# Performance work log

Hardware: AMD Instinct MI355X
Metric: run time of the kernel (lower is better)

Reference implementation:

```python
import jax, jax.numpy as jnp
import numpy as np

NUM_FEATURES = 512
NUM_HEADS = 8
DIM_PER_HEAD = NUM_FEATURES // NUM_HEADS


def setup_inputs() -> dict:
    key = jax.random.key(0)
    ks = jax.random.split(key, 9)
    B, C, H, W = 8, NUM_FEATURES, 32, 32
    # xavier_uniform bound for 1x1 conv: sqrt(6/(fan_in+fan_out)) = sqrt(6/(2C))
    bound = float(np.sqrt(6.0 / (2.0 * C)))
    # conv bias default init: U(-1/sqrt(fan_in), 1/sqrt(fan_in))
    bbound = float(1.0 / np.sqrt(C))
    return {
        "query": jax.random.normal(ks[0], (B, C, H, W), jnp.float32),
        "key": jax.random.normal(ks[1], (B, C, H, W), jnp.float32),
        "value": jax.random.normal(ks[2], (B, C, H, W), jnp.float32),
        "wq": jax.random.uniform(ks[3], (C, C), jnp.float32, -bound, bound),
        "bq": jax.random.uniform(ks[4], (C,), jnp.float32, -bbound, bbound),
        "wk": jax.random.uniform(ks[5], (C, C), jnp.float32, -bound, bound),
        "bk": jax.random.uniform(ks[6], (C,), jnp.float32, -bbound, bbound),
        "wv": jax.random.uniform(ks[7], (C, C), jnp.float32, -bound, bound),
        "bv": jax.random.uniform(ks[8], (C,), jnp.float32, -bbound, bbound),
    }


def _proj(x, w, b):
    # 1x1 conv == per-pixel linear over channels. x: [B,C,H,W], w: [Cout,Cin]
    return jnp.einsum('oi,bihw->bohw', w, x) + b[None, :, None, None]


def _split_heads(x, nh, d):
    B, C, H, W = x.shape
    # view (B, nh, d, H*W) then permute -> (B, nh, S, d)
    return x.reshape(B, nh, d, H * W).transpose(0, 1, 3, 2)


def reference(query, key, value, wq, bq, wk, bk, wv, bv):
    B, C, H, W = query.shape
    nh, d = NUM_HEADS, DIM_PER_HEAD
    q = _split_heads(_proj(query, wq, bq), nh, d)   # [B,nh,S,d]
    k = _split_heads(_proj(key, wk, bk), nh, d)
    v = _split_heads(_proj(value, wv, bv), nh, d)
    scores = jnp.einsum('bhsd,bhtd->bhst', q, k) / jnp.sqrt(jnp.float32(d))
    attn = jax.nn.softmax(scores, axis=-1)          # [B,nh,S,S]
    out = jnp.einsum('bhst,bhtd->bhsd', attn, v)    # [B,nh,S,d]
    # combine_heads (faithful to torch): permute to (B,S,nh,d), flat reshape
    out = out.transpose(0, 2, 1, 3)                 # [B,S,nh,d]
    return out.reshape(B, C, H, W)
```

## Files before the change

### kernel.cpp

```cpp
#include <hip/hip_runtime.h>
#include <hip/hip_bf16.h>
#include <stdint.h>


typedef __attribute__((ext_vector_type(4))) float f32x4;
typedef __attribute__((ext_vector_type(8))) short short8;
typedef __attribute__((ext_vector_type(4))) unsigned int u32x4;

#define GLB_AS(p) ((const __attribute__((address_space(1))) void*)(p))
#define LDS_AS(p) ((__attribute__((address_space(3))) void*)(p))

__device__ __forceinline__ unsigned short f2b(float f) {
  unsigned int x = __builtin_bit_cast(unsigned int, f);
  x = (x + 0x7FFFu + ((x >> 16) & 1u)) >> 16;
  return (unsigned short)x;
}

__device__ __forceinline__ float exp2_hw(float x) {
  float r;
  asm("v_exp_f32 %0, %1" : "=v"(r) : "v"(x));
  return r;
}

__device__ __forceinline__ unsigned int cvtpk(float lo, float hi) {
  unsigned int r;
  asm("v_cvt_pk_bf16_f32 %0, %1, %2" : "=v"(r) : "v"(lo), "v"(hi));
  return r;
}

__device__ __forceinline__ f32x4 mfma16(short8 a, short8 b, f32x4 c) {
  return __builtin_amdgcn_mfma_f32_16x16x32_bf16(a, b, c, 0, 0, 0);
}

__global__ __launch_bounds__(256) void prep_all(const float* __restrict__ Xq,
                                                const float* __restrict__ Xk,
                                                const float* __restrict__ Xv,
                                                const float* __restrict__ wq,
                                                const float* __restrict__ wk,
                                                const float* __restrict__ wv,
                                                unsigned short* __restrict__ Xt,
                                                unsigned short* __restrict__ WO) {
  __shared__ float t[64][65];
  const int tid = threadIdx.x;
  if (blockIdx.z == 24) {
    const int bid = blockIdx.y * 16 + blockIdx.x;
#pragma unroll
    for (int k = 0; k < 6; ++k) {
      int i = bid * 1536 + k * 256 + tid;
      int which = i >> 16, off = i & 65535;
      const float* W = (which == 0) ? wq : ((which == 1) ? wk : wv);
      float4 v = ((const float4*)W)[off];
      uint2 u;
      u.x = (unsigned)f2b(v.x) | ((unsigned)f2b(v.y) << 16);
      u.y = (unsigned)f2b(v.z) | ((unsigned)f2b(v.w) << 16);
      ((uint2*)(WO + (long)which * 262144))[off] = u;
    }
    return;
  }
  const int which = blockIdx.z >> 3, bb = blockIdx.z & 7;
  const float* X = (which == 0) ? Xq : ((which == 1) ? Xk : Xv);
  const int s0 = blockIdx.x * 64, c0 = blockIdx.y * 64;
  const float* Xb = X + (long)bb * 512 * 1024;
  const int col4 = (tid & 15) * 4;
  const int r0 = tid >> 4;
#pragma unroll
  for (int it = 0; it < 4; ++it) {
    int r = r0 + it * 16;
    const float4 v = *(const float4*)&Xb[(long)(c0 + r) * 1024 + s0 + col4];
    t[r][col4 + 0] = v.x; t[r][col4 + 1] = v.y; t[r][col4 + 2] = v.z; t[r][col4 + 3] = v.w;
  }
  __syncthreads();
  const int s = tid >> 2;
  const int cp = (tid & 3) * 16;
  unsigned int u[8];
#pragma unroll
  for (int i = 0; i < 8; ++i) {
    unsigned int lo = f2b(t[cp + 2 * i][s]);
    unsigned int hi = f2b(t[cp + 2 * i + 1][s]);
    u[i] = lo | (hi << 16);
  }
  unsigned short* dst = Xt + (long)which * 8 * 1024 * 512 +
                        ((long)bb * 1024 + s0 + s) * 512 + c0 + cp;
  ((uint4*)dst)[0] = make_uint4(u[0], u[1], u[2], u[3]);
  ((uint4*)dst)[1] = make_uint4(u[4], u[5], u[6], u[7]);
}

__global__ __launch_bounds__(256, 2) void gemm_proj(
    const unsigned short* __restrict__ XT, const unsigned short* __restrict__ W3,
    unsigned short* __restrict__ QKV, const float* __restrict__ bq,
    const float* __restrict__ bk, const float* __restrict__ bv) {
  __shared__ __align__(16) unsigned short lA[128 * 64];
  __shared__ __align__(16) unsigned short lB[128 * 64];
  const long SC = 1024L * 512;
  const int bid = blockIdx.x;
  const int kind = bid >> 8;
  const int rr = bid & 255;
  const int batch = rr >> 5, tile = rr & 31;
  const unsigned short *Ab, *Bb;
  unsigned short* Cb;
  const float* bias;
  int m0, n0, N, biasN;
  float scale = 1.0f;
  if (kind < 2) {
    m0 = (tile >> 2) * 128; n0 = (tile & 3) * 128; N = 512; biasN = 1;
    Ab = XT + ((long)kind * 8 + batch) * SC;
    Bb = W3 + (long)kind * 262144;
    Cb = QKV + ((long)kind * 8 + batch) * SC;
    bias = kind ? bk : bq;
    if (kind == 0) scale = 0.18033688011112042f;
  } else {
    m0 = (tile >> 3) * 128; n0 = (tile & 7) * 128; N = 1024; biasN = 0;
    Ab = W3 + 2 * 262144;
    Bb = XT + (16L + batch) * SC;
    Cb = QKV + (16L + batch) * SC;
    bias = bv;
  }
  const int tid = threadIdx.x, lane = tid & 63, wid = tid >> 6;
  const int wr = wid >> 1, wc = wid & 1;
  const int lm = lane & 15, lg = lane >> 4;
  f32x4 acc[4][4] = {};
  for (int k0 = 0; k0 < 512; k0 += 64) {
#pragma unroll
    for (int ch = wid; ch < 16; ch += 4) {
      int e = ch * 512 + lane * 8;
      int r = e >> 6, cc = e & 63;
      __builtin_amdgcn_global_load_lds(GLB_AS(Ab + (long)(m0 + r) * 512 + k0 + cc),
                                       LDS_AS(lA + ch * 512), 16, 0, 0);
      __builtin_amdgcn_global_load_lds(GLB_AS(Bb + (long)(n0 + r) * 512 + k0 + cc),
                                       LDS_AS(lB + ch * 512), 16, 0, 0);
    }
    __syncthreads();
#pragma unroll
    for (int kk = 0; kk < 2; ++kk) {
      short8 af[4], bf[4];
#pragma unroll
      for (int i = 0; i < 4; ++i)
        af[i] = *(const short8*)&lA[(wr * 64 + i * 16 + lm) * 64 + kk * 32 + 8 * lg];
#pragma unroll
      for (int j = 0; j < 4; ++j)
        bf[j] = *(const short8*)&lB[(wc * 64 + j * 16 + lm) * 64 + kk * 32 + 8 * lg];
#pragma unroll
      for (int i = 0; i < 4; ++i)
#pragma unroll
        for (int j = 0; j < 4; ++j)
          acc[i][j] = mfma16(af[i], bf[j], acc[i][j]);
    }
    __syncthreads();
  }
#pragma unroll
  for (int i = 0; i < 4; ++i)
#pragma unroll
    for (int j = 0; j < 4; ++j)
#pragma unroll
      for (int r = 0; r < 4; ++r) {
        int m = m0 + wr * 64 + i * 16 + lg * 4 + r;
        int n = n0 + wc * 64 + j * 16 + lm;
        float bvv = biasN ? bias[n] : bias[m];
        Cb[(long)m * N + n] = f2b((acc[i][j][r] + bvv) * scale);
      }
}

__global__ __launch_bounds__(256, 2) void attn(
    const unsigned short* __restrict__ Qt, const unsigned short* __restrict__ Kt,
    const unsigned short* __restrict__ V, float* __restrict__ Out) {
  __shared__ __align__(16) unsigned short lK[2][128 * 64];
  __shared__ __align__(16) unsigned short lV[2][64 * 128];
  const int flat = blockIdx.x;
  const int xcd = flat & 7, j = flat >> 3;
  const int pair = xcd * 8 + (j >> 3);
  const int st = j & 7;
  const int b = pair >> 3, h = pair & 7;
  const int tid = threadIdx.x, lane = tid & 63, w = tid >> 6;
  const int lm = lane & 15, lg = lane >> 4;
  const int s0 = st * 128 + w * 32;
  const unsigned short* Qb = Qt + ((long)b * 1024 + s0) * 512 + h * 64;
  const unsigned short* Kb = Kt + (long)b * 1024 * 512 + h * 64;
  const unsigned short* Vb = V + ((long)b * 512 + h * 64) * 1024;

  const int kscol = ((lane & 7) ^ (lane >> 3)) * 8;
  auto stage = [&](int buf, int t0) {
#pragma unroll
    for (int jj = 0; jj < 4; ++jj) {
      int ch = w * 4 + jj;
      int krow = ch * 8 + (lane >> 3);
      __builtin_amdgcn_global_load_lds(GLB_AS(Kb + (long)(t0 + krow) * 512 + kscol),
                                       LDS_AS(&lK[buf][ch * 512]), 16, 0, 0);
      int vrow = ch * 4 + (lane >> 4);
      int vcb = (lane & 15) ^ (vrow & 15);
      __builtin_amdgcn_global_load_lds(GLB_AS(Vb + (long)vrow * 1024 + t0 + vcb * 8),
                                       LDS_AS(&lV[buf][ch * 512]), 16, 0, 0);
    }
  };

  short8 qf[2][2];
#pragma unroll
  for (int si = 0; si < 2; ++si)
#pragma unroll
    for (int kk = 0; kk < 2; ++kk)
      qf[si][kk] = *(const short8*)&Qb[(si * 16 + lm) * 512 + kk * 32 + 8 * lg];

  f32x4 o[2][4] = {};
  float lsum[2] = {};

  stage(0, 0);
  __syncthreads();

#pragma unroll 1
  for (int t = 0; t < 8; ++t) {
    const int cur = t & 1;
    if (t < 7) stage(cur ^ 1, (t + 1) * 128);
    f32x4 s[2][8] = {};
    __builtin_amdgcn_s_setprio(1);
#pragma unroll
    for (int tj = 0; tj < 8; ++tj) {
      short8 kf0 = *(const short8*)&lK[cur][(tj * 16 + lm) * 64 + 8 * (lg ^ (lm & 7))];
      short8 kf1 = *(const short8*)&lK[cur][(tj * 16 + lm) * 64 + 8 * ((lg + 4) ^ (lm & 7))];
#pragma unroll
      for (int si = 0; si < 2; ++si) {
        s[si][tj] = mfma16(kf0, qf[si][0], s[si][tj]);
        s[si][tj] = mfma16(kf1, qf[si][1], s[si][tj]);
      }
    }
    __builtin_amdgcn_s_setprio(0);
#pragma unroll
    for (int si = 0; si < 2; ++si)
#pragma unroll
      for (int tj = 0; tj < 8; ++tj)
#pragma unroll
        for (int r = 0; r < 4; ++r) {
          float p = exp2_hw(s[si][tj][r]);
          s[si][tj][r] = p;
          lsum[si] += p;
        }
#pragma unroll
    for (int tk = 0; tk < 4; ++tk) {
      short8 pa[2];
#pragma unroll
      for (int si = 0; si < 2; ++si) {
        unsigned int X01 = cvtpk(s[si][2 * tk][0], s[si][2 * tk][1]);
        unsigned int X23 = cvtpk(s[si][2 * tk][2], s[si][2 * tk][3]);
        unsigned int Y01 = cvtpk(s[si][2 * tk + 1][0], s[si][2 * tk + 1][1]);
        unsigned int Y23 = cvtpk(s[si][2 * tk + 1][2], s[si][2 * tk + 1][3]);
        asm("v_permlane32_swap_b32 %0, %1" : "+v"(X01), "+v"(Y01));
        asm("v_permlane32_swap_b32 %0, %1" : "+v"(X23), "+v"(Y23));
        asm("v_permlane16_swap_b32 %0, %1" : "+v"(X01), "+v"(Y01));
        asm("v_permlane16_swap_b32 %0, %1" : "+v"(X23), "+v"(Y23));
        u32x4 pw;
        pw[0] = X01;
        pw[1] = X23;
        pw[2] = Y01;
        pw[3] = Y23;
        pa[si] = __builtin_bit_cast(short8, pw);
      }
      __builtin_amdgcn_s_setprio(1);
#pragma unroll
      for (int dj = 0; dj < 4; ++dj) {
        short8 vf = *(const short8*)&lV[cur][(dj * 16 + lm) * 128 + 8 * ((tk * 4 + lg) ^ lm)];
        o[0][dj] = mfma16(pa[0], vf, o[0][dj]);
        o[1][dj] = mfma16(pa[1], vf, o[1][dj]);
      }
      __builtin_amdgcn_s_setprio(0);
    }
    __syncthreads();
  }

  float inv[2][4];
#pragma unroll
  for (int si = 0; si < 2; ++si) {
    float rs = lsum[si];
    rs += __shfl_xor(rs, 16);
    rs += __shfl_xor(rs, 32);
#pragma unroll
    for (int r = 0; r < 4; ++r)
      inv[si][r] = 1.0f / __shfl(rs, lg * 4 + r);
  }
#pragma unroll
  for (int si = 0; si < 2; ++si)
#pragma unroll
    for (int dj = 0; dj < 4; ++dj)
#pragma unroll
      for (int r = 0; r < 4; ++r) {
        int srow2 = s0 + si * 16 + lg * 4 + r;
        Out[((long)b * 1024 + srow2) * 512 + h * 64 + dj * 16 + lm] = o[si][dj][r] * inv[si][r];
      }
}

extern "C" void kernel_launch(void* const* d_in, const int* in_sizes, int n_in,
                              void* d_out, int out_size, void* d_ws, size_t ws_size,
                              hipStream_t stream) {
  const float* query = (const float*)d_in[0];
  const float* key   = (const float*)d_in[1];
  const float* value = (const float*)d_in[2];
  const float* wq = (const float*)d_in[3];
  const float* bq = (const float*)d_in[4];
  const float* wk = (const float*)d_in[5];
  const float* bk = (const float*)d_in[6];
  const float* wv = (const float*)d_in[7];
  const float* bv = (const float*)d_in[8];

  unsigned short* ws = (unsigned short*)d_ws;
  const long SC = 1024L * 512;
  unsigned short* XT  = ws;
  unsigned short* W3  = XT + 24 * SC;
  unsigned short* QKV = W3 + 3 * 262144;
  unsigned short* QT  = QKV;
  unsigned short* KTm = QKV + 8 * SC;
  unsigned short* VVm = QKV + 16 * SC;

  prep_all<<<dim3(16, 8, 25), 256, 0, stream>>>(query, key, value, wq, wk, wv, XT, W3);
  gemm_proj<<<768, 256, 0, stream>>>(XT, W3, QKV, bq, bk, bv);
  attn<<<512, 256, 0, stream>>>(QT, KTm, VVm, (float*)d_out);
}
```

Baseline: 65.18 us.

## Halve attention tiles to 64 queries and 64 keys, doubling grid size

The attention kernel now processes 64 query rows per block (16 per wave) and iterates over 64-key tiles instead of 128, launching 1024 blocks instead of 512. LDS per block drops and the V staging swizzle is reworked for 64-wide rows. The aim is better occupancy and load balance across CUs, at the cost of less K/V reuse per block (twice the K/V traffic) and more loop iterations and barriers.

```diff
diff --git a/kernel.cpp b/kernel.cpp
--- a/kernel.cpp
+++ b/kernel.cpp
@@ -163,126 +163,108 @@
 __global__ __launch_bounds__(256, 2) void attn(
     const unsigned short* __restrict__ Qt, const unsigned short* __restrict__ Kt,
     const unsigned short* __restrict__ V, float* __restrict__ Out) {
-  __shared__ __align__(16) unsigned short lK[2][128 * 64];
-  __shared__ __align__(16) unsigned short lV[2][64 * 128];
+  __shared__ __align__(16) unsigned short lK[2][64 * 64];
+  __shared__ __align__(16) unsigned short lV[2][64 * 64];
   const int flat = blockIdx.x;
   const int xcd = flat & 7, j = flat >> 3;
-  const int pair = xcd * 8 + (j >> 3);
-  const int st = j & 7;
+  const int pair = xcd * 8 + (j >> 4);
+  const int st = j & 15;
   const int b = pair >> 3, h = pair & 7;
   const int tid = threadIdx.x, lane = tid & 63, w = tid >> 6;
   const int lm = lane & 15, lg = lane >> 4;
-  const int s0 = st * 128 + w * 32;
+  const int s0 = st * 64 + w * 16;
   const unsigned short* Qb = Qt + ((long)b * 1024 + s0) * 512 + h * 64;
   const unsigned short* Kb = Kt + (long)b * 1024 * 512 + h * 64;
   const unsigned short* Vb = V + ((long)b * 512 + h * 64) * 1024;
 
-  const int kscol = ((lane & 7) ^ (lane >> 3)) * 8;
+  const int srow = (w << 1) * 8 + (lane >> 3);
+  const int scol = ((lane & 7) ^ (lane >> 3)) * 8;
   auto stage = [&](int buf, int t0) {
 #pragma unroll
-    for (int jj = 0; jj < 4; ++jj) {
-      int ch = w * 4 + jj;
-      int krow = ch * 8 + (lane >> 3);
-      __builtin_amdgcn_global_load_lds(GLB_AS(Kb + (long)(t0 + krow) * 512 + kscol),
+    for (int jj = 0; jj < 2; ++jj) {
+      int ch = (w << 1) + jj;
+      int row = srow + jj * 8;
+      __builtin_amdgcn_global_load_lds(GLB_AS(Kb + (long)(t0 + row) * 512 + scol),
                                        LDS_AS(&lK[buf][ch * 512]), 16, 0, 0);
-      int vrow = ch * 4 + (lane >> 4);
-      int vcb = (lane & 15) ^ (vrow & 15);
-      __builtin_amdgcn_global_load_lds(GLB_AS(Vb + (long)vrow * 1024 + t0 + vcb * 8),
+      __builtin_amdgcn_global_load_lds(GLB_AS(Vb + (long)row * 1024 + t0 + scol),
                                        LDS_AS(&lV[buf][ch * 512]), 16, 0, 0);
     }
   };
 
-  short8 qf[2][2];
-#pragma unroll
-  for (int si = 0; si < 2; ++si)
-#pragma unroll
-    for (int kk = 0; kk < 2; ++kk)
-      qf[si][kk] = *(const short8*)&Qb[(si * 16 + lm) * 512 + kk * 32 + 8 * lg];
-
-  f32x4 o[2][4] = {};
-  float lsum[2] = {};
+  short8 qf[2];
+#pragma unroll
+  for (int kk = 0; kk < 2; ++kk)
+    qf[kk] = *(const short8*)&Qb[lm * 512 + kk * 32 + 8 * lg];
+
+  f32x4 o[4] = {};
+  float lsum = 0.f;
 
   stage(0, 0);
   __syncthreads();
 
 #pragma unroll 1
-  for (int t = 0; t < 8; ++t) {
+  for (int t = 0; t < 16; ++t) {
     const int cur = t & 1;
-    if (t < 7) stage(cur ^ 1, (t + 1) * 128);
-    f32x4 s[2][8] = {};
+    if (t < 15) stage(cur ^ 1, (t + 1) * 64);
+    f32x4 s[4] = {};
     __builtin_amdgcn_s_setprio(1);
 #pragma unroll
-    for (int tj = 0; tj < 8; ++tj) {
+    for (int tj = 0; tj < 4; ++tj) {
       short8 kf0 = *(const short8*)&lK[cur][(tj * 16 + lm) * 64 + 8 * (lg ^ (lm & 7))];
       short8 kf1 = *(const short8*)&lK[cur][(tj * 16 + lm) * 64 + 8 * ((lg + 4) ^ (lm & 7))];
-#pragma unroll
-      for (int si = 0; si < 2; ++si) {
-        s[si][tj] = mfma16(kf0, qf[si][0], s[si][tj]);
-        s[si][tj] = mfma16(kf1, qf[si][1], s[si][tj]);
+      s[tj] = mfma16(kf0, qf[0], s[tj]);
+      s[tj] = mfma16(kf1, qf[1], s[tj]);
+    }
+    __builtin_amdgcn_s_setprio(0);
+#pragma unroll
+    for (int tj = 0; tj < 4; ++tj)
+#pragma unroll
+      for (int r = 0; r < 4; ++r) {
+        float p = exp2_hw(s[tj][r]);
+        s[tj][r] = p;
+        lsum += p;
       }
-    }
-    __builtin_amdgcn_s_setprio(0);
-#pragma unroll
-    for (int si = 0; si < 2; ++si)
-#pragma unroll
-      for (int tj = 0; tj < 8; ++tj)
-#pragma unroll
-        for (int r = 0; r < 4; ++r) {
-          float p = exp2_hw(s[si][tj][r]);
-          s[si][tj][r] = p;
-          lsum[si] += p;
-        }
-#pragma unroll
-    for (int tk = 0; tk < 4; ++tk) {
-      short8 pa[2];
-#pragma unroll
-      for (int si = 0; si < 2; ++si) {
-        unsigned int X01 = cvtpk(s[si][2 * tk][0], s[si][2 * tk][1]);
-        unsigned int X23 = cvtpk(s[si][2 * tk][2], s[si][2 * tk][3]);
-        unsigned int Y01 = cvtpk(s[si][2 * tk + 1][0], s[si][2 * tk + 1][1]);
-        unsigned int Y23 = cvtpk(s[si][2 * tk + 1][2], s[si][2 * tk + 1][3]);
-        asm("v_permlane32_swap_b32 %0, %1" : "+v"(X01), "+v"(Y01));
-        asm("v_permlane32_swap_b32 %0, %1" : "+v"(X23), "+v"(Y23));
-        asm("v_permlane16_swap_b32 %0, %1" : "+v"(X01), "+v"(Y01));
-        asm("v_permlane16_swap_b32 %0, %1" : "+v"(X23), "+v"(Y23));
-        u32x4 pw;
-        pw[0] = X01;
-        pw[1] = X23;
-        pw[2] = Y01;
-        pw[3] = Y23;
-        pa[si] = __builtin_bit_cast(short8, pw);
-      }
+#pragma unroll
+    for (int tk = 0; tk < 2; ++tk) {
+      unsigned int X01 = cvtpk(s[2 * tk][0], s[2 * tk][1]);
+      unsigned int X23 = cvtpk(s[2 * tk][2], s[2 * tk][3]);
+      unsigned int Y01 = cvtpk(s[2 * tk + 1][0], s[2 * tk + 1][1]);
+      unsigned int Y23 = cvtpk(s[2 * tk + 1][2], s[2 * tk + 1][3]);
+      asm("v_permlane32_swap_b32 %0, %1" : "+v"(X01), "+v"(Y01));
+      asm("v_permlane32_swap_b32 %0, %1" : "+v"(X23), "+v"(Y23));
+      asm("v_permlane16_swap_b32 %0, %1" : "+v"(X01), "+v"(Y01));
+      asm("v_permlane16_swap_b32 %0, %1" : "+v"(X23), "+v"(Y23));
+      u32x4 pw;
+      pw[0] = X01;
+      pw[1] = X23;
+      pw[2] = Y01;
+      pw[3] = Y23;
+      short8 pa = __builtin_bit_cast(short8, pw);
       __builtin_amdgcn_s_setprio(1);
 #pragma unroll
       for (int dj = 0; dj < 4; ++dj) {
-        short8 vf = *(const short8*)&lV[cur][(dj * 16 + lm) * 128 + 8 * ((tk * 4 + lg) ^ lm)];
-        o[0][dj] = mfma16(pa[0], vf, o[0][dj]);
-        o[1][dj] = mfma16(pa[1], vf, o[1][dj]);
+        short8 vf = *(const short8*)&lV[cur][(dj * 16 + lm) * 64 + 8 * ((tk * 4 + lg) ^ (lm & 7))];
+        o[dj] = mfma16(pa, vf, o[dj]);
       }
       __builtin_amdgcn_s_setprio(0);
     }
     __syncthreads();
   }
 
-  float inv[2][4];
-#pragma unroll
-  for (int si = 0; si < 2; ++si) {
-    float rs = lsum[si];
-    rs += __shfl_xor(rs, 16);
-    rs += __shfl_xor(rs, 32);
-#pragma unroll
-    for (int r = 0; r < 4; ++r)
-      inv[si][r] = 1.0f / __shfl(rs, lg * 4 + r);
-  }
-#pragma unroll
-  for (int si = 0; si < 2; ++si)
-#pragma unroll
-    for (int dj = 0; dj < 4; ++dj)
-#pragma unroll
-      for (int r = 0; r < 4; ++r) {
-        int srow2 = s0 + si * 16 + lg * 4 + r;
-        Out[((long)b * 1024 + srow2) * 512 + h * 64 + dj * 16 + lm] = o[si][dj][r] * inv[si][r];
-      }
+  float rs = lsum;
+  rs += __shfl_xor(rs, 16);
+  rs += __shfl_xor(rs, 32);
+  float inv[4];
+#pragma unroll
+  for (int r = 0; r < 4; ++r)
+    inv[r] = 1.0f / __shfl(rs, lg * 4 + r);
+#pragma unroll
+  for (int dj = 0; dj < 4; ++dj)
+#pragma unroll
+    for (int r = 0; r < 4; ++r) {
+      int srow2 = s0 + lg * 4 + r;
+      Out[((long)b * 1024 + srow2) * 512 + h * 64 + dj * 16 + lm] = o[dj][r] * inv[r];
+    }
 }
 
 extern "C" void kernel_launch(void* const* d_in, const int* in_sizes, int n_in,
@@ -309,5 +291,5 @@
 
   prep_all<<<dim3(16, 8, 25), 256, 0, stream>>>(query, key, value, wq, wk, wv, XT, W3);
   gemm_proj<<<768, 256, 0, stream>>>(XT, W3, QKV, bq, bk, bv);
-  attn<<<512, 256, 0, stream>>>(QT, KTm, VVm, (float*)d_out);
-}
+  attn<<<1024, 256, 0, stream>>>(QT, KTm, VVm, (float*)d_out);
+}
```

Result: slower. 67.29 us (+3.2%).

## Fuse activation transpose and bf16 cast into projection GEMM with register prefetch

Applied to the files above, without the earlier changes.

The separate prep pass that transposed fp32 activations into a bf16 workspace is removed. The projection GEMM now reads fp32 X directly, converts it in registers and writes swizzled bf16 tiles into LDS, double-buffering the global loads in registers across k-steps. Weights are still cast by a small separate kernel. This removes a full write and re-read of the transposed activation buffer, at the cost of more register pressure and dropping the launch_bounds occupancy hint. The block order is also reindexed so that batch varies fastest.

```diff
diff --git a/kernel.cpp b/kernel.cpp
--- a/kernel.cpp
+++ b/kernel.cpp
@@ -32,131 +32,134 @@
   return __builtin_amdgcn_mfma_f32_16x16x32_bf16(a, b, c, 0, 0, 0);
 }
 
-__global__ __launch_bounds__(256) void prep_all(const float* __restrict__ Xq,
-                                                const float* __restrict__ Xk,
-                                                const float* __restrict__ Xv,
-                                                const float* __restrict__ wq,
-                                                const float* __restrict__ wk,
-                                                const float* __restrict__ wv,
-                                                unsigned short* __restrict__ Xt,
-                                                unsigned short* __restrict__ WO) {
-  __shared__ float t[64][65];
-  const int tid = threadIdx.x;
-  if (blockIdx.z == 24) {
-    const int bid = blockIdx.y * 16 + blockIdx.x;
-#pragma unroll
-    for (int k = 0; k < 6; ++k) {
-      int i = bid * 1536 + k * 256 + tid;
-      int which = i >> 16, off = i & 65535;
-      const float* W = (which == 0) ? wq : ((which == 1) ? wk : wv);
-      float4 v = ((const float4*)W)[off];
-      uint2 u;
-      u.x = (unsigned)f2b(v.x) | ((unsigned)f2b(v.y) << 16);
-      u.y = (unsigned)f2b(v.z) | ((unsigned)f2b(v.w) << 16);
-      ((uint2*)(WO + (long)which * 262144))[off] = u;
-    }
-    return;
-  }
-  const int which = blockIdx.z >> 3, bb = blockIdx.z & 7;
-  const float* X = (which == 0) ? Xq : ((which == 1) ? Xk : Xv);
-  const int s0 = blockIdx.x * 64, c0 = blockIdx.y * 64;
-  const float* Xb = X + (long)bb * 512 * 1024;
-  const int col4 = (tid & 15) * 4;
-  const int r0 = tid >> 4;
-#pragma unroll
-  for (int it = 0; it < 4; ++it) {
-    int r = r0 + it * 16;
-    const float4 v = *(const float4*)&Xb[(long)(c0 + r) * 1024 + s0 + col4];
-    t[r][col4 + 0] = v.x; t[r][col4 + 1] = v.y; t[r][col4 + 2] = v.z; t[r][col4 + 3] = v.w;
-  }
-  __syncthreads();
-  const int s = tid >> 2;
-  const int cp = (tid & 3) * 16;
-  unsigned int u[8];
-#pragma unroll
-  for (int i = 0; i < 8; ++i) {
-    unsigned int lo = f2b(t[cp + 2 * i][s]);
-    unsigned int hi = f2b(t[cp + 2 * i + 1][s]);
-    u[i] = lo | (hi << 16);
-  }
-  unsigned short* dst = Xt + (long)which * 8 * 1024 * 512 +
-                        ((long)bb * 1024 + s0 + s) * 512 + c0 + cp;
-  ((uint4*)dst)[0] = make_uint4(u[0], u[1], u[2], u[3]);
-  ((uint4*)dst)[1] = make_uint4(u[4], u[5], u[6], u[7]);
-}
-
-__global__ __launch_bounds__(256, 2) void gemm_proj(
-    const unsigned short* __restrict__ XT, const unsigned short* __restrict__ W3,
-    unsigned short* __restrict__ QKV, const float* __restrict__ bq,
-    const float* __restrict__ bk, const float* __restrict__ bv) {
+__global__ __launch_bounds__(256) void cast_w3(const float* __restrict__ wq,
+                                               const float* __restrict__ wk,
+                                               const float* __restrict__ wv,
+                                               unsigned short* __restrict__ O) {
+  const int y = blockIdx.y;
+  const float* W = (y == 0) ? wq : ((y == 1) ? wk : wv);
+  int i = blockIdx.x * 256 + threadIdx.x;
+  float4 v = ((const float4*)W)[i];
+  uint2 u;
+  u.x = (unsigned)f2b(v.x) | ((unsigned)f2b(v.y) << 16);
+  u.y = (unsigned)f2b(v.z) | ((unsigned)f2b(v.w) << 16);
+  ((uint2*)(O + (long)y * 262144))[i] = u;
+}
+
+__global__ void gemm_proj(const float* __restrict__ Xq, const float* __restrict__ Xk,
+                          const float* __restrict__ Xv, const unsigned short* __restrict__ W3,
+                          unsigned short* __restrict__ QKV, const float* __restrict__ bq,
+                          const float* __restrict__ bk, const float* __restrict__ bv) {
   __shared__ __align__(16) unsigned short lA[128 * 64];
   __shared__ __align__(16) unsigned short lB[128 * 64];
   const long SC = 1024L * 512;
   const int bid = blockIdx.x;
-  const int kind = bid >> 8;
-  const int rr = bid & 255;
-  const int batch = rr >> 5, tile = rr & 31;
-  const unsigned short *Ab, *Bb;
+  const int batch = bid & 7;
+  const int j = bid >> 3;
+  const int kind = j >> 5, tile = j & 31;
+  const bool aFromX = (kind < 2);
+  const float* Xsrc = ((kind == 0) ? Xq : ((kind == 1) ? Xk : Xv)) + (long)batch * 512 * 1024;
+  const unsigned short* Wsrc = W3 + (long)kind * 262144;
   unsigned short* Cb;
   const float* bias;
-  int m0, n0, N, biasN;
+  int m0, n0, N, biasN, r0x, wrow0;
   float scale = 1.0f;
-  if (kind < 2) {
+  if (aFromX) {
     m0 = (tile >> 2) * 128; n0 = (tile & 3) * 128; N = 512; biasN = 1;
-    Ab = XT + ((long)kind * 8 + batch) * SC;
-    Bb = W3 + (long)kind * 262144;
+    r0x = m0; wrow0 = n0;
     Cb = QKV + ((long)kind * 8 + batch) * SC;
     bias = kind ? bk : bq;
     if (kind == 0) scale = 0.18033688011112042f;
   } else {
     m0 = (tile >> 3) * 128; n0 = (tile & 7) * 128; N = 1024; biasN = 0;
-    Ab = W3 + 2 * 262144;
-    Bb = XT + (16L + batch) * SC;
+    r0x = n0; wrow0 = m0;
     Cb = QKV + (16L + batch) * SC;
     bias = bv;
   }
+  unsigned short* lX = aFromX ? lA : lB;
+  unsigned short* lW = aFromX ? lB : lA;
   const int tid = threadIdx.x, lane = tid & 63, wid = tid >> 6;
   const int wr = wid >> 1, wc = wid & 1;
   const int lm = lane & 15, lg = lane >> 4;
-  f32x4 acc[4][4] = {};
-  for (int k0 = 0; k0 < 512; k0 += 64) {
+  const int aX = aFromX ? (lm & 7) : 0;
+  const int bX = aFromX ? 0 : (lm & 7);
+  const int oct = lane & 7, qd = lane >> 3;
+  const int xrow = wid * 32 + qd * 4;
+
+  auto loadX = [&](f32x4 (&v)[8], int k0) {
+#pragma unroll
+    for (int e = 0; e < 8; ++e)
+      v[e] = *(const f32x4*)&Xsrc[(long)(k0 + oct * 8 + e) * 1024 + r0x + xrow];
+  };
+  auto writeX = [&](f32x4 (&v)[8]) {
+#pragma unroll
+    for (int jj = 0; jj < 4; ++jj) {
+      int row = xrow + jj;
+      u32x4 pw;
+      pw[0] = cvtpk(v[0][jj], v[1][jj]);
+      pw[1] = cvtpk(v[2][jj], v[3][jj]);
+      pw[2] = cvtpk(v[4][jj], v[5][jj]);
+      pw[3] = cvtpk(v[6][jj], v[7][jj]);
+      *(u32x4*)&lX[row * 64 + 8 * (oct ^ (row & 7))] = pw;
+    }
+  };
+  auto stageW = [&](int k0) {
 #pragma unroll
     for (int ch = wid; ch < 16; ch += 4) {
       int e = ch * 512 + lane * 8;
       int r = e >> 6, cc = e & 63;
-      __builtin_amdgcn_global_load_lds(GLB_AS(Ab + (long)(m0 + r) * 512 + k0 + cc),
-                                       LDS_AS(lA + ch * 512), 16, 0, 0);
-      __builtin_amdgcn_global_load_lds(GLB_AS(Bb + (long)(n0 + r) * 512 + k0 + cc),
-                                       LDS_AS(lB + ch * 512), 16, 0, 0);
-    }
-    __syncthreads();
+      __builtin_amdgcn_global_load_lds(GLB_AS(Wsrc + (long)(wrow0 + r) * 512 + k0 + cc),
+                                       LDS_AS(lW + ch * 512), 16, 0, 0);
+    }
+  };
+
+  f32x4 acc[4][4] = {};
+  auto compute = [&]() {
 #pragma unroll
     for (int kk = 0; kk < 2; ++kk) {
       short8 af[4], bf[4];
 #pragma unroll
       for (int i = 0; i < 4; ++i)
-        af[i] = *(const short8*)&lA[(wr * 64 + i * 16 + lm) * 64 + kk * 32 + 8 * lg];
-#pragma unroll
-      for (int j = 0; j < 4; ++j)
-        bf[j] = *(const short8*)&lB[(wc * 64 + j * 16 + lm) * 64 + kk * 32 + 8 * lg];
+        af[i] = *(const short8*)&lA[(wr * 64 + i * 16 + lm) * 64 + 8 * ((kk * 4 + lg) ^ aX)];
+#pragma unroll
+      for (int jj = 0; jj < 4; ++jj)
+        bf[jj] = *(const short8*)&lB[(wc * 64 + jj * 16 + lm) * 64 + 8 * ((kk * 4 + lg) ^ bX)];
 #pragma unroll
       for (int i = 0; i < 4; ++i)
 #pragma unroll
-        for (int j = 0; j < 4; ++j)
-          acc[i][j] = mfma16(af[i], bf[j], acc[i][j]);
-    }
+        for (int jj = 0; jj < 4; ++jj)
+          acc[i][jj] = mfma16(af[i], bf[jj], acc[i][jj]);
+    }
+  };
+
+  f32x4 vA[8], vB[8];
+  loadX(vA, 0);
+#pragma unroll 1
+  for (int kq = 0; kq < 8; kq += 2) {
+    stageW(kq * 64);
+    loadX(vB, kq * 64 + 64);
+    writeX(vA);
+    __syncthreads();
+    compute();
+    __syncthreads();
+    stageW(kq * 64 + 64);
+    if (kq < 6) loadX(vA, kq * 64 + 128);
+    writeX(vB);
+    __syncthreads();
+    compute();
     __syncthreads();
   }
+
 #pragma unroll
   for (int i = 0; i < 4; ++i)
 #pragma unroll
-    for (int j = 0; j < 4; ++j)
+    for (int jj = 0; jj < 4; ++jj)
 #pragma unroll
       for (int r = 0; r < 4; ++r) {
         int m = m0 + wr * 64 + i * 16 + lg * 4 + r;
-        int n = n0 + wc * 64 + j * 16 + lm;
+        int n = n0 + wc * 64 + jj * 16 + lm;
         float bvv = biasN ? bias[n] : bias[m];
-        Cb[(long)m * N + n] = f2b((acc[i][j][r] + bvv) * scale);
+        Cb[(long)m * N + n] = f2b((acc[i][jj][r] + bvv) * scale);
       }
 }
 
@@ -300,14 +303,13 @@
 
   unsigned short* ws = (unsigned short*)d_ws;
   const long SC = 1024L * 512;
-  unsigned short* XT  = ws;
-  unsigned short* W3  = XT + 24 * SC;
+  unsigned short* W3  = ws;
   unsigned short* QKV = W3 + 3 * 262144;
   unsigned short* QT  = QKV;
   unsigned short* KTm = QKV + 8 * SC;
   unsigned short* VVm = QKV + 16 * SC;
 
-  prep_all<<<dim3(16, 8, 25), 256, 0, stream>>>(query, key, value, wq, wk, wv, XT, W3);
-  gemm_proj<<<768, 256, 0, stream>>>(XT, W3, QKV, bq, bk, bv);
+  cast_w3<<<dim3(256, 3), 256, 0, stream>>>(wq, wk, wv, W3);
+  gemm_proj<<<768, 256, 0, stream>>>(query, key, value, W3, QKV, bq, bk, bv);
   attn<<<512, 256, 0, stream>>>(QT, KTm, VVm, (float*)d_out);
 }
```

After: 129.1 us. 1.98x slower.
